# Kernel optimization log

Measured on AMD Instinct MI355X. Metric: run time of the kernel, lower is better.

The kernel has to match this reference:

```python
import jax, jax.numpy as jnp
import numpy as np

MAX_DEPTH = 6
NUM_TREES = 64
LEAF_DIMS = 128
D_IN = 512
BATCH = 4096
N_INTERNAL = 2 ** MAX_DEPTH - 1  # 63
N_LEAVES = 2 ** MAX_DEPTH        # 64


def setup_inputs() -> dict:
    key = jax.random.key(0)
    ks = jax.random.split(key, 4)
    x = jax.random.normal(ks[0], (BATCH, D_IN), dtype=jnp.float32)
    # Stacked internal-node dense layers, node i at index i (level order, node_index ordering)
    W = jax.random.normal(ks[1], (N_INTERNAL, D_IN, NUM_TREES), dtype=jnp.float32) / np.sqrt(D_IN)
    b = jnp.zeros((N_INTERNAL, NUM_TREES), dtype=jnp.float32)
    leaf_weight = jax.random.normal(ks[2], (N_LEAVES, LEAF_DIMS, NUM_TREES), dtype=jnp.float32)
    gates = jax.random.normal(ks[3], (N_LEAVES, LEAF_DIMS, NUM_TREES), dtype=jnp.float32)
    return {"x": x, "W": W, "b": b, "leaf_weight": leaf_weight, "gates": gates}


def reference(x, W, b, leaf_weight, gates):
    # All internal-node gating probabilities in one batched matmul:
    # g[b, n, t] = sigmoid(x[b] @ W[n] + b[n])  for every internal node n, tree t
    g = jax.nn.sigmoid(jnp.einsum('bd,ndt->bnt', x, W) + b[None, :, :])  # [B, 63, T]

    B = x.shape[0]
    T = W.shape[-1]
    # Path probability to each leaf, built level by level.
    # Level l has 2^l nodes at internal indices [2^l - 1, 2^(l+1) - 2];
    # interleaving (left=p*g, right=p*(1-g)) matches node_index child ordering.
    p = jnp.ones((B, 1, T), dtype=x.dtype)
    for level in range(MAX_DEPTH):
        start = 2 ** level - 1
        n_lvl = 2 ** level
        gl = g[:, start:start + n_lvl, :]                  # [B, n_lvl, T]
        children = jnp.stack([p * gl, p * (1.0 - gl)], axis=2)  # [B, n_lvl, 2, T]
        p = children.reshape(B, 2 * n_lvl, T)
    # p: [B, n_leaves, T] leaf path probabilities

    # Softmax mixture-of-experts gate over trees, then weighted leaf mixture:
    # out[b, d] = sum_{l, t} p[b, l, t] * leaf_weight[l, d, t] * softmax(gates, -1)[l, d, t]
    w = leaf_weight * jax.nn.softmax(gates, axis=-1)  # [L, D, T]
    out = jnp.einsum('blt,ldt->bd', p, w)
    return out
```

## Files before the change

### kernel.cpp

```cpp
#include <hip/hip_runtime.h>
#include <stdint.h>

#define BATCH 4096
#define DIN   512
#define NT    64
#define NL    64
#define LD    128

typedef __attribute__((ext_vector_type(8))) short bf16x8;
typedef __attribute__((ext_vector_type(8))) _Float16 f16x8;
typedef __attribute__((ext_vector_type(4))) float f32x4;

typedef const __attribute__((address_space(1))) unsigned char* gcp_t;
typedef __attribute__((address_space(3))) unsigned char* lp_t;

__device__ __forceinline__ void gl_lds16(const void* g, void* l) {
  __builtin_amdgcn_global_load_lds((gcp_t)g, (lp_t)l, 16, 0, 0);
}

__device__ __forceinline__ unsigned short f2bf(float f) {
  union { float f; unsigned u; } a; a.f = f;
  unsigned r = a.u + 0x7FFFu + ((a.u >> 16) & 1u);
  return (unsigned short)(r >> 16);
}

__global__ __launch_bounds__(256) void prep_all_k(
    const float* __restrict__ x, const float* __restrict__ W,
    const float* __restrict__ gates, const float* __restrict__ lw,
    unsigned short* __restrict__ xb, unsigned short* __restrict__ Wt,
    unsigned short* __restrict__ Wv2) {
  __shared__ float smem[12288];
  const int bx = blockIdx.x;
  const int tid = threadIdx.x;

  if (bx < 2048) {
    int i = bx * 256 + tid;
    float4 v = ((const float4*)x)[i];
    ushort4 o;
    o.x = f2bf(v.x); o.y = f2bf(v.y); o.z = f2bf(v.z); o.w = f2bf(v.w);
    ((ushort4*)xb)[i] = o;
  } else if (bx < 2304) {
    int bb = bx - 2048;
    int n = bb >> 2, d0 = (bb & 3) * 128;
    float* buf = smem;
    if (n < 63) {
      for (int it = 0; it < 32; ++it) {
        int idx = it * 256 + tid;
        buf[idx] = W[n * 32768 + (d0 + (idx >> 6)) * 64 + (idx & 63)];
      }
    }
    __syncthreads();
    int t = tid >> 2, q = tid & 3;
    unsigned short vals[32];
    #pragma unroll
    for (int j = 0; j < 32; ++j)
      vals[j] = (n < 63) ? f2bf(buf[(q * 32 + j) * 64 + t]) : (unsigned short)0;
    uint4* dst = (uint4*)(Wt + t * 32768 + n * 512 + d0 + q * 32);
    const uint4* src = (const uint4*)vals;
    dst[0] = src[0]; dst[1] = src[1]; dst[2] = src[2]; dst[3] = src[3];
  } else {
    int d = bx - 2304;
    float* gb = smem;
    float* lb = smem + 4096;
    float* wv = smem + 8192;
    for (int it = 0; it < 16; ++it) {
      int idx = it * 256 + tid;
      int l = idx >> 6;
      int ga = l * 8192 + d * 64 + (idx & 63);
      gb[idx] = gates[ga];
      lb[idx] = lw[ga];
    }
    __syncthreads();
    int wave = tid >> 6, lane = tid & 63;
    for (int l = wave; l < 64; l += 4) {
      float v = gb[l * 64 + lane];
      float mx = v;
      for (int m = 32; m >= 1; m >>= 1) mx = fmaxf(mx, __shfl_xor(mx, m));
      float e = __expf(v - mx);
      float s = e;
      for (int m = 32; m >= 1; m >>= 1) s += __shfl_xor(s, m);
      wv[l * 64 + lane] = lb[l * 64 + lane] * e / s;
    }
    __syncthreads();
    #pragma unroll
    for (int c = 0; c < 2; ++c) {
      int k0 = tid * 16 + c * 8;
      union { unsigned short u[8]; uint4 v; } o;
      #pragma unroll
      for (int j = 0; j < 8; ++j) {
        int k = k0 + j;
        o.u[j] = f2bf(wv[(k & 63) * 64 + (k >> 6)]);
      }
      *(uint4*)(Wv2 + (long)d * 4096 + k0) = o.v;
    }
  }
}

__global__ __launch_bounds__(256, 4) void gemm1_tree_k(
    const unsigned short* __restrict__ xb,
    const unsigned short* __restrict__ Wt,
    const float* __restrict__ bias,
    unsigned short* __restrict__ P)
{
  __shared__ __align__(16) char smem[34816];
  __shared__ float bb[128];
  unsigned short* AsB = (unsigned short*)smem;
  unsigned short* BsB = (unsigned short*)(smem + 16384);
  _Float16* gbuf = (_Float16*)smem;

  const int tid = threadIdx.x;
  const int wave = tid >> 6, lane = tid & 63;
  const int b0 = blockIdx.x * 128;
  const int t0 = blockIdx.y * 2;

  if (tid < 128) {
    int n = tid & 63, t = t0 + (tid >> 6);
    bb[tid] = (n < 63) ? bias[n * 64 + t] : 0.0f;
  }

  const f32x4 zero = {0.f, 0.f, 0.f, 0.f};
  f32x4 acc[4][4];
  #pragma unroll
  for (int i = 0; i < 4; ++i)
    #pragma unroll
    for (int j = 0; j < 4; ++j) acc[i][j] = zero;

  const int g0 = wave * 64 + lane;
  const int g1 = g0 + 256;
  const unsigned short* Ag0 = xb + (long)(b0 + (g0 >> 2)) * 512 + (g0 & 3) * 8;
  const unsigned short* Ag1 = xb + (long)(b0 + (g1 >> 2)) * 512 + (g1 & 3) * 8;
  const unsigned short* Bg0 = Wt + (long)(t0 * 64 + (g0 >> 2)) * 512 + (g0 & 3) * 8;
  const unsigned short* Bg1 = Wt + (long)(t0 * 64 + (g1 >> 2)) * 512 + (g1 & 3) * 8;
  const int lofs0 = wave * 512;
  const int lofs1 = wave * 512 + 2048;

  const int wm = (wave >> 1) * 64, wn = (wave & 1) * 64;
  const int mrow = lane & 15, kg = lane >> 4;

  gl_lds16(Ag0, AsB + lofs0);
  gl_lds16(Ag1, AsB + lofs1);
  gl_lds16(Bg0, BsB + lofs0);
  gl_lds16(Bg1, BsB + lofs1);

  for (int it = 0; it < 16; ++it) {
    const int buf = (it & 1) * 4096;
    if (it < 15) {
      const int kk = (it + 1) * 32;
      const int nbuf = ((it + 1) & 1) * 4096;
      gl_lds16(Ag0 + kk, AsB + nbuf + lofs0);
      gl_lds16(Ag1 + kk, AsB + nbuf + lofs1);
      gl_lds16(Bg0 + kk, BsB + nbuf + lofs0);
      gl_lds16(Bg1 + kk, BsB + nbuf + lofs1);
      asm volatile("s_waitcnt vmcnt(4)" ::: "memory");
    } else {
      asm volatile("s_waitcnt vmcnt(0)" ::: "memory");
    }
    asm volatile("s_barrier" ::: "memory");

    bf16x8 fa[4], fb[4];
    #pragma unroll
    for (int i = 0; i < 4; ++i)
      fa[i] = *(const bf16x8*)(AsB + buf + (wm + i * 16 + mrow) * 32 + kg * 8);
    #pragma unroll
    for (int j = 0; j < 4; ++j)
      fb[j] = *(const bf16x8*)(BsB + buf + (wn + j * 16 + mrow) * 32 + kg * 8);
    #pragma unroll
    for (int i = 0; i < 4; ++i)
      #pragma unroll
      for (int j = 0; j < 4; ++j)
        acc[i][j] = __builtin_amdgcn_mfma_f32_16x16x32_bf16(fa[i], fb[j], acc[i][j], 0, 0, 0);

    asm volatile("s_waitcnt lgkmcnt(0)" ::: "memory");
    asm volatile("s_barrier" ::: "memory");
  }

  #pragma unroll
  for (int i = 0; i < 4; ++i)
    #pragma unroll
    for (int j = 0; j < 4; ++j) {
      int col = wn + j * 16 + mrow;
      float bv = bb[col];
      #pragma unroll
      for (int r = 0; r < 4; ++r) {
        int row = wm + i * 16 + kg * 4 + r;
        float z = acc[i][j][r] + bv;
        gbuf[row * 136 + col] = (_Float16)(1.0f / (1.0f + __expf(-z)));
      }
    }
  __syncthreads();

  {
    const int row = tid >> 1, tr = tid & 1;
    const _Float16* grow = gbuf + row * 136 + tr * 64;
    float g[63];
    #pragma unroll
    for (int c = 0; c < 8; ++c) {
      f16x8 gv = *(const f16x8*)(grow + c * 8);
      #pragma unroll
      for (int j = 0; j < 8; ++j) {
        int n = c * 8 + j;
        if (n < 63) g[n] = (float)gv[j];
      }
    }
    float P3[8];
    {
      float a0 = g[0],            a1 = 1.0f - g[0];
      float c0 = a0 * g[1],       c1 = a0 * (1.0f - g[1]);
      float c2 = a1 * g[2],       c3 = a1 * (1.0f - g[2]);
      P3[0] = c0 * g[3];  P3[1] = c0 * (1.0f - g[3]);
      P3[2] = c1 * g[4];  P3[3] = c1 * (1.0f - g[4]);
      P3[4] = c2 * g[5];  P3[5] = c2 * (1.0f - g[5]);
      P3[6] = c3 * g[6];  P3[7] = c3 * (1.0f - g[6]);
    }
    unsigned short* prow = P + (long)(b0 + row) * 4096 + (t0 + tr) * 64;
    #pragma unroll
    for (int o = 0; o < 8; ++o) {
      float g3 = g[7 + o];
      float q0 = P3[o] * g3, q1 = P3[o] * (1.0f - g3);
      float g4a = g[15 + 2 * o], g4b = g[16 + 2 * o];
      float r0 = q0 * g4a, r1 = q0 * (1.0f - g4a);
      float r2 = q1 * g4b, r3 = q1 * (1.0f - g4b);
      union { unsigned short u[8]; uint4 v; } ou;
      #pragma unroll
      for (int h = 0; h < 4; ++h) {
        float g5 = g[31 + 4 * o + h];
        float rr = (h == 0) ? r0 : (h == 1) ? r1 : (h == 2) ? r2 : r3;
        ou.u[2 * h]     = f2bf(rr * g5);
        ou.u[2 * h + 1] = f2bf(rr * (1.0f - g5));
      }
      *(uint4*)(prow + o * 8) = ou.v;
    }
  }
}

__global__ __launch_bounds__(256, 4) void gemm2_k(
    const unsigned short* __restrict__ P,
    const unsigned short* __restrict__ Wv2,
    float* __restrict__ out)
{
  __shared__ unsigned short AsB[2][64 * 32];
  __shared__ unsigned short BsB[2][128 * 32];
  const int tid = threadIdx.x;
  const int wave = tid >> 6, lane = tid & 63;
  const int b0 = blockIdx.x * 64;
  const int k0 = blockIdx.y * 256;

  const f32x4 zero = {0.f, 0.f, 0.f, 0.f};
  f32x4 acc[2][4];
  #pragma unroll
  for (int i = 0; i < 2; ++i)
    #pragma unroll
    for (int j = 0; j < 4; ++j) acc[i][j] = zero;

  const int g0 = wave * 64 + lane;
  const int g1 = g0 + 256;
  const unsigned short* Ag0 = P + (long)(b0 + (g0 >> 2)) * 4096 + k0 + (g0 & 3) * 8;
  const unsigned short* Bg0 = Wv2 + (long)(g0 >> 2) * 4096 + k0 + (g0 & 3) * 8;
  const unsigned short* Bg1 = Wv2 + (long)(g1 >> 2) * 4096 + k0 + (g1 & 3) * 8;
  const int lofs = wave * 512;

  const int wm = (wave >> 1) * 32, wn = (wave & 1) * 64;
  const int mrow = lane & 15, kg = lane >> 4;

  gl_lds16(Ag0, AsB[0] + lofs);
  gl_lds16(Bg0, BsB[0] + lofs);
  gl_lds16(Bg1, BsB[0] + lofs + 2048);

  for (int it = 0; it < 8; ++it) {
    const int buf = it & 1;
    if (it < 7) {
      const int kk = (it + 1) * 32;
      const int nbuf = (it + 1) & 1;
      gl_lds16(Ag0 + kk, AsB[nbuf] + lofs);
      gl_lds16(Bg0 + kk, BsB[nbuf] + lofs);
      gl_lds16(Bg1 + kk, BsB[nbuf] + lofs + 2048);
      asm volatile("s_waitcnt vmcnt(3)" ::: "memory");
    } else {
      asm volatile("s_waitcnt vmcnt(0)" ::: "memory");
    }
    asm volatile("s_barrier" ::: "memory");

    bf16x8 fa[2], fb[4];
    #pragma unroll
    for (int i = 0; i < 2; ++i)
      fa[i] = *(const bf16x8*)(AsB[buf] + (wm + i * 16 + mrow) * 32 + kg * 8);
    #pragma unroll
    for (int j = 0; j < 4; ++j)
      fb[j] = *(const bf16x8*)(BsB[buf] + (wn + j * 16 + mrow) * 32 + kg * 8);
    #pragma unroll
    for (int i = 0; i < 2; ++i)
      #pragma unroll
      for (int j = 0; j < 4; ++j)
        acc[i][j] = __builtin_amdgcn_mfma_f32_16x16x32_bf16(fa[i], fb[j], acc[i][j], 0, 0, 0);

    asm volatile("s_waitcnt lgkmcnt(0)" ::: "memory");
    asm volatile("s_barrier" ::: "memory");
  }

  #pragma unroll
  for (int i = 0; i < 2; ++i)
    #pragma unroll
    for (int j = 0; j < 4; ++j) {
      int col = wn + j * 16 + mrow;
      #pragma unroll
      for (int r = 0; r < 4; ++r) {
        int row = wm + i * 16 + kg * 4 + r;
        atomicAdd(&out[(long)(b0 + row) * 128 + col], acc[i][j][r]);
      }
    }
}

extern "C" void kernel_launch(void* const* d_in, const int* in_sizes, int n_in,
                              void* d_out, int out_size, void* d_ws, size_t ws_size,
                              hipStream_t stream) {
  const float* x     = (const float*)d_in[0];
  const float* W     = (const float*)d_in[1];
  const float* b     = (const float*)d_in[2];
  const float* lw    = (const float*)d_in[3];
  const float* gates = (const float*)d_in[4];
  float* out = (float*)d_out;

  char* ws = (char*)d_ws;
  unsigned short* xb  = (unsigned short*)(ws);
  unsigned short* Wt  = (unsigned short*)(ws + (4l  << 20));
  unsigned short* Wv2 = (unsigned short*)(ws + (8l  << 20));
  unsigned short* P   = (unsigned short*)(ws + (16l << 20));

  hipMemsetAsync(out, 0, (size_t)4096 * 128 * sizeof(float), stream);
  hipLaunchKernelGGL(prep_all_k,   dim3(2432),   dim3(256), 0, stream,
                     x, W, gates, lw, xb, Wt, Wv2);
  hipLaunchKernelGGL(gemm1_tree_k, dim3(32, 32), dim3(256), 0, stream, xb, Wt, b, P);
  hipLaunchKernelGGL(gemm2_k,      dim3(64, 16), dim3(256), 0, stream, P, Wv2, out);
}
```

Measured before the change: 154.5 us.

## Pack bf16 conversions with perm, use rcp sigmoid, cut gemm2 split-K

Replaces round-to-nearest-even bf16 conversion with a cheaper round-half-up conversion that packs two values per perm instruction. This is used in prep, the tree path output and the weight prep. The sigmoid now uses a hardware reciprocal instead of a division. gemm2's split-K factor drops from 16 to 4, with each block covering 1024 K, which reduces atomic accumulation traffic into out at the cost of fewer blocks (256). Rounding changes slightly, with ties no longer going to even.

```diff
diff --git a/kernel.cpp b/kernel.cpp
--- a/kernel.cpp
+++ b/kernel.cpp
@@ -18,10 +18,15 @@
   __builtin_amdgcn_global_load_lds((gcp_t)g, (lp_t)l, 16, 0, 0);
 }
 
+__device__ __forceinline__ unsigned pk_bf16(float a, float b) {
+  union { float f; unsigned u; } ua, ub;
+  ua.f = a; ub.f = b;
+  return __builtin_amdgcn_perm(ub.u + 0x8000u, ua.u + 0x8000u, 0x07060302u);
+}
+
 __device__ __forceinline__ unsigned short f2bf(float f) {
   union { float f; unsigned u; } a; a.f = f;
-  unsigned r = a.u + 0x7FFFu + ((a.u >> 16) & 1u);
-  return (unsigned short)(r >> 16);
+  return (unsigned short)((a.u + 0x8000u) >> 16);
 }
 
 __global__ __launch_bounds__(256) void prep_all_k(
@@ -36,9 +41,10 @@
   if (bx < 2048) {
     int i = bx * 256 + tid;
     float4 v = ((const float4*)x)[i];
-    ushort4 o;
-    o.x = f2bf(v.x); o.y = f2bf(v.y); o.z = f2bf(v.z); o.w = f2bf(v.w);
-    ((ushort4*)xb)[i] = o;
+    uint2 o;
+    o.x = pk_bf16(v.x, v.y);
+    o.y = pk_bf16(v.z, v.w);
+    ((uint2*)xb)[i] = o;
   } else if (bx < 2304) {
     int bb = bx - 2048;
     int n = bb >> 2, d0 = (bb & 3) * 128;
@@ -51,10 +57,13 @@
     }
     __syncthreads();
     int t = tid >> 2, q = tid & 3;
-    unsigned short vals[32];
-    #pragma unroll
-    for (int j = 0; j < 32; ++j)
-      vals[j] = (n < 63) ? f2bf(buf[(q * 32 + j) * 64 + t]) : (unsigned short)0;
+    unsigned vals[16];
+    #pragma unroll
+    for (int j = 0; j < 16; ++j) {
+      float va = (n < 63) ? buf[(q * 32 + 2 * j) * 64 + t] : 0.0f;
+      float vb = (n < 63) ? buf[(q * 32 + 2 * j + 1) * 64 + t] : 0.0f;
+      vals[j] = (n < 63) ? pk_bf16(va, vb) : 0u;
+    }
     uint4* dst = (uint4*)(Wt + t * 32768 + n * 512 + d0 + q * 32);
     const uint4* src = (const uint4*)vals;
     dst[0] = src[0]; dst[1] = src[1]; dst[2] = src[2]; dst[3] = src[3];
@@ -85,13 +94,13 @@
     #pragma unroll
     for (int c = 0; c < 2; ++c) {
       int k0 = tid * 16 + c * 8;
-      union { unsigned short u[8]; uint4 v; } o;
-      #pragma unroll
-      for (int j = 0; j < 8; ++j) {
-        int k = k0 + j;
-        o.u[j] = f2bf(wv[(k & 63) * 64 + (k >> 6)]);
-      }
-      *(uint4*)(Wv2 + (long)d * 4096 + k0) = o.v;
+      unsigned o[4];
+      #pragma unroll
+      for (int j = 0; j < 4; ++j) {
+        int ka = k0 + 2 * j, kb = k0 + 2 * j + 1;
+        o[j] = pk_bf16(wv[(ka & 63) * 64 + (ka >> 6)], wv[(kb & 63) * 64 + (kb >> 6)]);
+      }
+      *(uint4*)(Wv2 + (long)d * 4096 + k0) = *(const uint4*)o;
     }
   }
 }
@@ -184,7 +193,7 @@
       for (int r = 0; r < 4; ++r) {
         int row = wm + i * 16 + kg * 4 + r;
         float z = acc[i][j][r] + bv;
-        gbuf[row * 136 + col] = (_Float16)(1.0f / (1.0f + __expf(-z)));
+        gbuf[row * 136 + col] = (_Float16)__builtin_amdgcn_rcpf(1.0f + __expf(-z));
       }
     }
   __syncthreads();
@@ -220,15 +229,14 @@
       float g4a = g[15 + 2 * o], g4b = g[16 + 2 * o];
       float r0 = q0 * g4a, r1 = q0 * (1.0f - g4a);
       float r2 = q1 * g4b, r3 = q1 * (1.0f - g4b);
-      union { unsigned short u[8]; uint4 v; } ou;
+      unsigned ou[4];
       #pragma unroll
       for (int h = 0; h < 4; ++h) {
         float g5 = g[31 + 4 * o + h];
         float rr = (h == 0) ? r0 : (h == 1) ? r1 : (h == 2) ? r2 : r3;
-        ou.u[2 * h]     = f2bf(rr * g5);
-        ou.u[2 * h + 1] = f2bf(rr * (1.0f - g5));
-      }
-      *(uint4*)(prow + o * 8) = ou.v;
+        ou[h] = pk_bf16(rr * g5, rr * (1.0f - g5));
+      }
+      *(uint4*)(prow + o * 8) = *(const uint4*)ou;
     }
   }
 }
@@ -243,7 +251,7 @@
   const int tid = threadIdx.x;
   const int wave = tid >> 6, lane = tid & 63;
   const int b0 = blockIdx.x * 64;
-  const int k0 = blockIdx.y * 256;
+  const int k0 = blockIdx.y * 1024;
 
   const f32x4 zero = {0.f, 0.f, 0.f, 0.f};
   f32x4 acc[2][4];
@@ -266,9 +274,9 @@
   gl_lds16(Bg0, BsB[0] + lofs);
   gl_lds16(Bg1, BsB[0] + lofs + 2048);
 
-  for (int it = 0; it < 8; ++it) {
+  for (int it = 0; it < 32; ++it) {
     const int buf = it & 1;
-    if (it < 7) {
+    if (it < 31) {
       const int kk = (it + 1) * 32;
       const int nbuf = (it + 1) & 1;
       gl_lds16(Ag0 + kk, AsB[nbuf] + lofs);
@@ -330,5 +338,5 @@
   hipLaunchKernelGGL(prep_all_k,   dim3(2432),   dim3(256), 0, stream,
                      x, W, gates, lw, xb, Wt, Wv2);
   hipLaunchKernelGGL(gemm1_tree_k, dim3(32, 32), dim3(256), 0, stream, xb, Wt, b, P);
-  hipLaunchKernelGGL(gemm2_k,      dim3(64, 16), dim3(256), 0, stream, P, Wv2, out);
-}
+  hipLaunchKernelGGL(gemm2_k,      dim3(64, 4),  dim3(256), 0, stream, P, Wv2, out);
+}
```

After: 140.3 us. 9.2% less time.
